# Performance work log

Hardware: AMD Instinct MI355X
Metric: run time of the kernel (lower is better)

## Reference

```python
import jax, jax.numpy as jnp
import numpy as np

N = 50000        # nodes
E = 800000       # edges
H = 256          # hidden_dim == output_dim
L = 5            # num_layers
NUM_ATOM_F = 9   # OGB atom categorical features
NUM_BOND_F = 3   # OGB bond categorical features
ATOM_VOCAB = 64
BOND_VOCAB = 8
G = 128          # num graphs in batch
BN_EPS = 1e-5


def setup_inputs() -> dict:
    key = jax.random.key(0)
    ks = jax.random.split(key, 24)
    s = 0.02
    inp = {
        "x_feat": jax.random.randint(ks[0], (N, NUM_ATOM_F), 0, ATOM_VOCAB),
        "edge_index": jax.random.randint(ks[1], (2, E), 0, N),
        "edge_attr_raw": jax.random.randint(ks[2], (E, NUM_BOND_F), 0, BOND_VOCAB),
        "batch": jnp.sort(jax.random.randint(ks[3], (N,), 0, G)),
        "atom_emb": s * jax.random.normal(ks[4], (NUM_ATOM_F, ATOM_VOCAB, H), jnp.float32),
        "bond_emb": s * jax.random.normal(ks[5], (NUM_BOND_F, BOND_VOCAB, H), jnp.float32),
        # per-layer GINEConv MLP: Linear(H,H) -> BN -> relu -> Linear(H,H) -> relu
        "W1": s * jax.random.normal(ks[6], (L, H, H), jnp.float32),
        "b1": jnp.zeros((L, H), jnp.float32),
        "g1": jnp.ones((L, H), jnp.float32),
        "be1": jnp.zeros((L, H), jnp.float32),
        "W2": s * jax.random.normal(ks[7], (L, H, H), jnp.float32),
        "b2": jnp.zeros((L, H), jnp.float32),
        # outer per-layer BN
        "g2": jnp.ones((L, H), jnp.float32),
        "be2": jnp.zeros((L, H), jnp.float32),
        # output head: Linear -> BN -> relu -> Linear
        "outW1": s * jax.random.normal(ks[8], (H, H), jnp.float32),
        "outb1": jnp.zeros((H,), jnp.float32),
        "outg": jnp.ones((H,), jnp.float32),
        "outbe": jnp.zeros((H,), jnp.float32),
        "outW2": s * jax.random.normal(ks[9], (H, H), jnp.float32),
        "outb2": jnp.zeros((H,), jnp.float32),
    }
    return inp


def _bn(x, g, b):
    mu = jnp.mean(x, axis=0)
    var = jnp.var(x, axis=0)
    return (x - mu) * jax.lax.rsqrt(var + BN_EPS) * g + b


def reference(x_feat, edge_index, edge_attr_raw, batch,
              atom_emb, bond_emb, W1, b1, g1, be1, W2, b2, g2, be2,
              outW1, outb1, outg, outbe, outW2, outb2):
    # Atom/Bond encoders: sum of per-feature embeddings
    x = sum(atom_emb[f][x_feat[:, f]] for f in range(NUM_ATOM_F))        # [N,H]
    e = sum(bond_emb[f][edge_attr_raw[:, f]] for f in range(NUM_BOND_F))  # [E,H]
    src, dst = edge_index[0], edge_index[1]

    for i in range(L):
        # GINEConv: (1+eps)*x + sum_j relu(x_j + e_ij), eps=0
        m = jax.nn.relu(x[src] + e)                       # [E,H]
        agg = jax.ops.segment_sum(m, dst, num_segments=N)  # [N,H]
        h = x + agg
        h = jax.nn.relu(_bn(h @ W1[i] + b1[i], g1[i], be1[i]))
        h = jax.nn.relu(h @ W2[i] + b2[i])
        x = jax.nn.relu(_bn(h, g2[i], be2[i]))

    # output head + global_add_pool
    h = jax.nn.relu(_bn(x @ outW1 + outb1, outg, outbe))
    h = h @ outW2 + outb2
    return jax.ops.segment_sum(h, batch, num_segments=G)   # [G,H]
```

## Files before the change

kernel.cpp:

```cpp
#include <hip/hip_runtime.h>
#include <hip/hip_bf16.h>

#define NN 50000
#define EE 800000
#define HH 256
#define GG 128
#define LL 5
#define NCHUNK 196
#define BN_EPS 1e-5f

typedef __attribute__((ext_vector_type(8))) short short8_t;
typedef __attribute__((ext_vector_type(4))) float f32x4;
typedef __hip_bfloat16 bf16;

#define AS1 __attribute__((address_space(1)))
#define AS3 __attribute__((address_space(3)))

__device__ __forceinline__ float bf2f(unsigned short u) {
    unsigned int i = ((unsigned int)u) << 16;
    float f;
    __builtin_memcpy(&f, &i, 4);
    return f;
}
__device__ __forceinline__ unsigned short f2bf(float f) {
    bf16 h = __float2bfloat16(f);
    unsigned short u;
    __builtin_memcpy(&u, &h, 2);
    return u;
}

__global__ __launch_bounds__(256) void k_encode(const int* __restrict__ xf,
                                                const float* __restrict__ atom_emb,
                                                bf16* __restrict__ x) {
    int n = blockIdx.x, h = threadIdx.x;
    float s = 0.f;
#pragma unroll
    for (int f = 0; f < 9; ++f) {
        int v = xf[n * 9 + f];
        s += atom_emb[((size_t)f * 64 + v) * HH + h];
    }
    x[(size_t)n * HH + h] = __float2bfloat16(s);
}

__global__ __launch_bounds__(256) void k_combo(const float* __restrict__ bond_emb,
                                               bf16* __restrict__ table) {
    int c = blockIdx.x, h = threadIdx.x;
    float v = bond_emb[(size_t)((c >> 6) & 7) * HH + h]
            + bond_emb[(size_t)(8 + ((c >> 3) & 7)) * HH + h]
            + bond_emb[(size_t)(16 + (c & 7)) * HH + h];
    table[(size_t)c * HH + h] = __float2bfloat16(v);
}

__global__ __launch_bounds__(256) void k_prepw(const float* __restrict__ W1,
                                               const float* __restrict__ W2,
                                               const float* __restrict__ oW1,
                                               const float* __restrict__ oW2,
                                               bf16* __restrict__ out) {
    int z = blockIdx.z;
    const float* src = (z < 5) ? W1 + (size_t)z * 65536
                     : (z < 10) ? W2 + (size_t)(z - 5) * 65536
                     : (z == 10) ? oW1 : oW2;
    bf16* dst = out + (size_t)z * 65536;
    __shared__ float tile[32][33];
    int kt = blockIdx.y * 32, nt = blockIdx.x * 32;
    int tx = threadIdx.x, ty = threadIdx.y;
    for (int i = ty; i < 32; i += 8) tile[i][tx] = src[(size_t)(kt + i) * 256 + nt + tx];
    __syncthreads();
    for (int i = ty; i < 32; i += 8)
        dst[(size_t)(nt + i) * 256 + kt + tx] = __float2bfloat16(tile[tx][i]);
}

__global__ __launch_bounds__(256) void k_hist(const int* __restrict__ ei, int* __restrict__ deg) {
    int e = blockIdx.x * 256 + threadIdx.x;
    if (e < EE) atomicAdd(&deg[ei[EE + e]], 1);
}

__global__ __launch_bounds__(256) void k_scan_a(const int* __restrict__ deg, int* __restrict__ ro,
                                                int* __restrict__ bsum) {
    __shared__ int sm[256];
    int b = blockIdx.x, t = threadIdx.x;
    int idx = b * 256 + t;
    int v = (idx < NN) ? deg[idx] : 0;
    sm[t] = v;
    __syncthreads();
    for (int off = 1; off < 256; off <<= 1) {
        int add = (t >= off) ? sm[t - off] : 0;
        __syncthreads();
        sm[t] += add;
        __syncthreads();
    }
    if (idx <= NN) ro[idx] = sm[t] - v;
    if (t == 255) bsum[b] = sm[255];
}

__global__ __launch_bounds__(256) void k_scan_b(int* __restrict__ bsum) {
    __shared__ int sm[256];
    int t = threadIdx.x;
    int v = (t < NCHUNK) ? bsum[t] : 0;
    sm[t] = v;
    __syncthreads();
    for (int off = 1; off < 256; off <<= 1) {
        int add = (t >= off) ? sm[t - off] : 0;
        __syncthreads();
        sm[t] += add;
        __syncthreads();
    }
    if (t < NCHUNK) bsum[t] = sm[t] - v;
}

__global__ __launch_bounds__(256) void k_scan_c(int* __restrict__ ro, const int* __restrict__ bsum,
                                                int* __restrict__ cursor) {
    int b = blockIdx.x, t = threadIdx.x;
    int idx = b * 256 + t;
    if (idx <= NN) {
        int val = ro[idx] + bsum[b];
        ro[idx] = val;
        if (idx < NN) cursor[idx] = val;
    }
}

__global__ __launch_bounds__(256) void k_scatter(const int* __restrict__ ei,
                                                 const int* __restrict__ attr,
                                                 int* __restrict__ cursor,
                                                 int2* __restrict__ ebuf) {
    int e = blockIdx.x * 256 + threadIdx.x;
    if (e < EE) {
        int d = ei[EE + e];
        int c = (attr[e * 3] << 6) | (attr[e * 3 + 1] << 3) | attr[e * 3 + 2];
        int pos = atomicAdd(&cursor[d], 1);
        ebuf[pos] = make_int2(ei[e], c);
    }
}

__global__ __launch_bounds__(256) void k_bnrelu(bf16* __restrict__ t,
                                                const float* __restrict__ sIn,
                                                const float* __restrict__ qIn,
                                                const float* __restrict__ gIn,
                                                const float* __restrict__ beIn,
                                                float invN) {
    int grp = threadIdx.x >> 6;
    int lane = threadIdx.x & 63;
    int h4 = lane * 4;
    float4 s4 = *(const float4*)(sIn + h4);
    float4 q4 = *(const float4*)(qIn + h4);
    float4 g4 = *(const float4*)(gIn + h4);
    float4 b4 = *(const float4*)(beIn + h4);
    float4 cav, cbv;
#define COEF(C)                                                 \
    { float mu = s4.C * invN;                                   \
      float var = fmaf(-mu, mu, q4.C * invN);                   \
      float a = g4.C * rsqrtf(var + BN_EPS);                    \
      cav.C = a; cbv.C = fmaf(-mu, a, b4.C); }
    COEF(x) COEF(y) COEF(z) COEF(w)
#undef COEF
    int n = blockIdx.x * 4 + grp;
    if (n >= NN) return;
    ushort4 v = *(const ushort4*)(t + (size_t)n * HH + h4);
    ushort4 o;
    o.x = f2bf(fmaxf(fmaf(bf2f(v.x), cav.x, cbv.x), 0.f));
    o.y = f2bf(fmaxf(fmaf(bf2f(v.y), cav.y, cbv.y), 0.f));
    o.z = f2bf(fmaxf(fmaf(bf2f(v.z), cav.z, cbv.z), 0.f));
    o.w = f2bf(fmaxf(fmaf(bf2f(v.w), cav.w, cbv.w), 0.f));
    *(ushort4*)(t + (size_t)n * HH + h4) = o;
}

__global__ __launch_bounds__(256) void k_aggregate(const bf16* __restrict__ u,
                                                   const int* __restrict__ ro,
                                                   const int2* __restrict__ eb,
                                                   const bf16* __restrict__ combo,
                                                   bf16* __restrict__ aggout) {
    int wid = threadIdx.x >> 6;
    int lane = threadIdx.x & 63;
    int half = lane >> 5;
    int sl = lane & 31;
    int n = blockIdx.x * 4 + wid;
    if (n >= NN) return;
    int h8 = sl * 8;
    float p0[8] = {0.f, 0.f, 0.f, 0.f, 0.f, 0.f, 0.f, 0.f};
    float p1[8] = {0.f, 0.f, 0.f, 0.f, 0.f, 0.f, 0.f, 0.f};
    int e0 = ro[n], e1 = ro[n + 1];
    int j = e0;
#define ACCUM(P, xs, cs)                                                       \
    {                                                                          \
        unsigned int xw[4] = {xs.x, xs.y, xs.z, xs.w};                         \
        unsigned int cw[4] = {cs.x, cs.y, cs.z, cs.w};                         \
        _Pragma("unroll") for (int q = 0; q < 4; ++q) {                        \
            float xlo = __uint_as_float(xw[q] << 16);                          \
            float xhi = __uint_as_float(xw[q] & 0xffff0000u);                  \
            float clo = __uint_as_float(cw[q] << 16);                          \
            float chi = __uint_as_float(cw[q] & 0xffff0000u);                  \
            P[2 * q] += fmaxf(xlo + clo, 0.f);                                 \
            P[2 * q + 1] += fmaxf(xhi + chi, 0.f);                             \
        }                                                                      \
    }
    for (; j + 4 <= e1; j += 4) {
        int2 rA = eb[j + half];
        int2 rB = eb[j + 2 + half];
        uint4 xA = *(const uint4*)(u + (size_t)rA.x * HH + h8);
        uint4 cA = *(const uint4*)(combo + ((size_t)rA.y << 8) + h8);
        uint4 xB = *(const uint4*)(u + (size_t)rB.x * HH + h8);
        uint4 cB = *(const uint4*)(combo + ((size_t)rB.y << 8) + h8);
        ACCUM(p0, xA, cA);
        ACCUM(p1, xB, cB);
    }
    for (; j < e1; j += 2) {
        int idx = j + half;
        bool v = idx < e1;
        int2 r = eb[v ? idx : e0];
        uint4 xA = *(const uint4*)(u + (size_t)r.x * HH + h8);
        uint4 cA = *(const uint4*)(combo + ((size_t)r.y << 8) + h8);
        if (v) ACCUM(p0, xA, cA);
    }
#undef ACCUM
#pragma unroll
    for (int i = 0; i < 8; ++i) {
        p0[i] += p1[i];
        p0[i] += __shfl_xor(p0[i], 32);
    }
    if (half == 0) {
        uint4 tv = *(const uint4*)(u + (size_t)n * HH + h8);
        unsigned int tw[4] = {tv.x, tv.y, tv.z, tv.w};
        unsigned int ow[4];
#pragma unroll
        for (int q = 0; q < 4; ++q) {
            float tlo = __uint_as_float(tw[q] << 16);
            float thi = __uint_as_float(tw[q] & 0xffff0000u);
            ow[q] = (unsigned int)f2bf(p0[2 * q] + tlo)
                  | ((unsigned int)f2bf(p0[2 * q + 1] + thi) << 16);
        }
        *(uint4*)(aggout + (size_t)n * HH + h8) = make_uint4(ow[0], ow[1], ow[2], ow[3]);
    }
}

struct GLds {
    uint4 a[2][512];
    uint4 b[2][1024];
    float ca[256], cb[256];
};

__device__ __forceinline__ uint4 xchunk(uint4 u, const float* ca, const float* cb, int k0) {
    float4 ca0 = *(const float4*)(ca + k0);
    float4 ca1 = *(const float4*)(ca + k0 + 4);
    float4 cb0 = *(const float4*)(cb + k0);
    float4 cb1 = *(const float4*)(cb + k0 + 4);
    float cav[8] = {ca0.x, ca0.y, ca0.z, ca0.w, ca1.x, ca1.y, ca1.z, ca1.w};
    float cbv[8] = {cb0.x, cb0.y, cb0.z, cb0.w, cb1.x, cb1.y, cb1.z, cb1.w};
    unsigned int s[4] = {u.x, u.y, u.z, u.w};
#pragma unroll
    for (int p = 0; p < 4; ++p) {
        float lo = bf2f((unsigned short)(s[p] & 0xffffu));
        float hi = bf2f((unsigned short)(s[p] >> 16));
        lo = fmaxf(fmaf(lo, cav[2 * p], cbv[2 * p]), 0.f);
        hi = fmaxf(fmaf(hi, cav[2 * p + 1], cbv[2 * p + 1]), 0.f);
        s[p] = (unsigned int)f2bf(lo) | ((unsigned int)f2bf(hi) << 16);
    }
    return make_uint4(s[0], s[1], s[2], s[3]);
}

template <bool HAS_T, bool POOL>
__global__ __launch_bounds__(512, 4) void k_gemm(const bf16* __restrict__ A,
                                                 const bf16* __restrict__ Wt,
                                                 const float* __restrict__ bias,
                                                 bf16* __restrict__ Out,
                                                 int M, int do_relu,
                                                 const float* __restrict__ sIn,
                                                 const float* __restrict__ qIn,
                                                 const float* __restrict__ gIn,
                                                 const float* __restrict__ beIn,
                                                 float invN,
                                                 float* __restrict__ ssum,
                                                 float* __restrict__ ssq,
                                                 const int* __restrict__ pbatch,
                                                 float* __restrict__ pout) {
    __shared__ GLds L;
    const int t = threadIdx.x;
    const int lane = t & 63;
    const int w = t >> 6;
    const int wr = w >> 2, wc = w & 3;
    const int m0 = blockIdx.x * 128;
    const int lhi = lane >> 4, llo = lane & 15;

    if (HAS_T) {
        if (t < 256) {
            float mu = sIn[t] * invN;
            float var = fmaf(-mu, mu, qIn[t] * invN);
            float a = gIn[t] * rsqrtf(var + BN_EPS);
            L.ca[t] = a;
            L.cb[t] = fmaf(-mu, a, beIn[t]);
        }
        __syncthreads();
    }

    const int arow_i = t & 127, akg = t >> 7;
    const bf16* aptr = A + (size_t)(m0 + arow_i) * HH + akg * 8;
    const int bcol = wc * 64 + lane;
    const bf16* bptr = Wt + (size_t)bcol * HH + wr * 8;

    f32x4 acc[4][4] = {};
    uint4 areg, anext;

#define STAGE_B(c, kb)                                                                        \
    _Pragma("unroll") for (int q = 0; q < 2; ++q) {                                           \
        __builtin_amdgcn_global_load_lds((const AS1 void*)(bptr + (kb) + q * 16),             \
                                         (AS3 void*)&L.b[c][q * 512 + w * 64], 16, 0, 0);     \
    }
#define STAGE_A_DMA(c, kb)                                                                    \
    __builtin_amdgcn_global_load_lds((const AS1 void*)(aptr + (kb)),                          \
                                     (AS3 void*)&L.a[c][w * 64], 16, 0, 0);

    STAGE_B(0, 0);
    if (HAS_T) {
        areg = *(const uint4*)(aptr + 0);
        L.a[0][t] = xchunk(areg, L.ca, L.cb, akg * 8);
    } else {
        STAGE_A_DMA(0, 0);
    }
    __syncthreads();

    int c = 0;
    for (int step = 0; step < 8; ++step) {
        const int kn = (step + 1) * 32;
        if (step < 7) {
            STAGE_B(c ^ 1, kn);
            if (HAS_T) anext = *(const uint4*)(aptr + kn);
            else STAGE_A_DMA(c ^ 1, kn);
        }
        short8_t af[4], bfv[4];
#pragma unroll
        for (int m = 0; m < 4; ++m)
            af[m] = *(const short8_t*)&L.a[c][lhi * 128 + wr * 64 + m * 16 + llo];
#pragma unroll
        for (int n = 0; n < 4; ++n)
            bfv[n] = *(const short8_t*)&L.b[c][lhi * 256 + wc * 64 + n * 16 + llo];
#pragma unroll
        for (int m = 0; m < 4; ++m)
#pragma unroll
            for (int n = 0; n < 4; ++n)
                acc[m][n] = __builtin_amdgcn_mfma_f32_16x16x32_bf16(af[m], bfv[n], acc[m][n], 0, 0, 0);
        if (HAS_T && step < 7)
            L.a[c ^ 1][t] = xchunk(anext, L.ca, L.cb, kn + akg * 8);
        __syncthreads();
        c ^= 1;
    }
#undef STAGE_B
#undef STAGE_A_DMA

    float bias_n[4];
    int col_n[4];
#pragma unroll
    for (int n = 0; n < 4; ++n) {
        col_n[n] = wc * 64 + n * 16 + llo;
        bias_n[n] = bias[col_n[n]];
    }

    if (POOL) {
        int gcur = -1;
        float pacc[4] = {0.f, 0.f, 0.f, 0.f};
#pragma unroll
        for (int m = 0; m < 4; ++m) {
#pragma unroll
            for (int j = 0; j < 4; ++j) {
                int row = m0 + wr * 64 + m * 16 + lhi * 4 + j;
                if (row < M) {
                    int g = pbatch[row];
                    if (g != gcur) {
                        if (gcur >= 0) {
#pragma unroll
                            for (int n = 0; n < 4; ++n)
                                atomicAdd(&pout[(size_t)gcur * HH + col_n[n]], pacc[n]);
                        }
                        gcur = g;
#pragma unroll
                        for (int n = 0; n < 4; ++n) pacc[n] = 0.f;
                    }
#pragma unroll
                    for (int n = 0; n < 4; ++n)
                        pacc[n] += acc[m][n][j] + bias_n[n];
                }
            }
        }
        if (gcur >= 0) {
#pragma unroll
            for (int n = 0; n < 4; ++n)
                atomicAdd(&pout[(size_t)gcur * HH + col_n[n]], pacc[n]);
        }
        return;
    }

    float ps[4] = {0.f, 0.f, 0.f, 0.f}, pq[4] = {0.f, 0.f, 0.f, 0.f};
#pragma unroll
    for (int m = 0; m < 4; ++m) {
#pragma unroll
        for (int j = 0; j < 4; ++j) {
            int row = m0 + wr * 64 + m * 16 + lhi * 4 + j;
            bool valid = row < M;
#pragma unroll
            for (int n = 0; n < 4; ++n) {
                float v = acc[m][n][j] + bias_n[n];
                if (do_relu) v = fmaxf(v, 0.f);
                if (valid) {
                    Out[(size_t)row * HH + col_n[n]] = __float2bfloat16(v);
                    ps[n] += v;
                    pq[n] = fmaf(v, v, pq[n]);
                }
            }
        }
    }

    if (ssum) {
#pragma unroll
        for (int n = 0; n < 4; ++n) {
            float s = ps[n];
            s += __shfl_xor(s, 16);
            s += __shfl_xor(s, 32);
            float q = pq[n];
            q += __shfl_xor(q, 16);
            q += __shfl_xor(q, 32);
            if (lhi == 0) {
                atomicAdd(&ssum[col_n[n]], s);
                atomicAdd(&ssq[col_n[n]], q);
            }
        }
    }
}

static size_t align256(size_t v) { return (v + 255) & ~(size_t)255; }

extern "C" void kernel_launch(void* const* d_in, const int* in_sizes, int n_in,
                              void* d_out, int out_size, void* d_ws, size_t ws_size,
                              hipStream_t stream) {
    const int* x_feat = (const int*)d_in[0];
    const int* ei = (const int*)d_in[1];
    const int* attr = (const int*)d_in[2];
    const int* batch = (const int*)d_in[3];
    const float* atom_emb = (const float*)d_in[4];
    const float* bond_emb = (const float*)d_in[5];
    const float* W1 = (const float*)d_in[6];
    const float* b1 = (const float*)d_in[7];
    const float* g1 = (const float*)d_in[8];
    const float* be1 = (const float*)d_in[9];
    const float* W2 = (const float*)d_in[10];
    const float* b2 = (const float*)d_in[11];
    const float* g2 = (const float*)d_in[12];
    const float* be2 = (const float*)d_in[13];
    const float* outW1 = (const float*)d_in[14];
    const float* outb1 = (const float*)d_in[15];
    const float* outg = (const float*)d_in[16];
    const float* outbe = (const float*)d_in[17];
    const float* outW2 = (const float*)d_in[18];
    const float* outb2 = (const float*)d_in[19];
    float* out = (float*)d_out;

    char* ws = (char*)d_ws;
    const size_t BUF_STRIDE = align256((size_t)NN * HH * 2 + 131072);
    bf16* bufA = (bf16*)ws;
    bf16* bufB = (bf16*)(ws + BUF_STRIDE);
    bf16* bufC = (bf16*)(ws + 2 * BUF_STRIDE);
    char* p = ws + 3 * BUF_STRIDE;
    int2* ebuf = (int2*)p;            p += align256((size_t)EE * sizeof(int2));
    int* deg = (int*)p;
    float* stats = (float*)(p + (size_t)NN * sizeof(int));
    const size_t ZERO_BYTES = (size_t)NN * sizeof(int) + 11 * 512 * sizeof(float);
    p += align256(ZERO_BYTES);
    int* ro = (int*)p;                p += align256((size_t)(NN + 1) * sizeof(int));
    int* cursor = (int*)p;            p += align256((size_t)NN * sizeof(int));
    int* bsum = (int*)p;              p += align256(256 * sizeof(int));
    bf16* combo = (bf16*)p;           p += align256((size_t)512 * HH * sizeof(bf16));
    bf16* wbuf = (bf16*)p;            p += align256((size_t)12 * 65536 * sizeof(bf16));

    const float invN = 1.0f / (float)NN;
    const int EBLK = (EE + 255) / 256;
    const int GBLK = (NN + 127) / 128;
    const int AGG_GRID = (NN + 3) / 4;
    const int BNR_GRID = (NN + 3) / 4;

    hipMemsetAsync(deg, 0, ZERO_BYTES, stream);
    hipMemsetAsync(d_out, 0, (size_t)GG * HH * sizeof(float), stream);
    k_hist<<<EBLK, 256, 0, stream>>>(ei, deg);
    k_scan_a<<<NCHUNK, 256, 0, stream>>>(deg, ro, bsum);
    k_scan_b<<<1, 256, 0, stream>>>(bsum);
    k_scan_c<<<NCHUNK, 256, 0, stream>>>(ro, bsum, cursor);
    k_scatter<<<EBLK, 256, 0, stream>>>(ei, attr, cursor, ebuf);
    k_combo<<<512, 256, 0, stream>>>(bond_emb, combo);
    k_prepw<<<dim3(8, 8, 12), dim3(32, 8), 0, stream>>>(W1, W2, outW1, outW2, wbuf);
    k_encode<<<NN, 256, 0, stream>>>(x_feat, atom_emb, bufA);

    for (int l = 0; l < LL; ++l) {
        float* s1 = stats + (size_t)(2 * l) * 512;
        float* q1 = s1 + 256;
        float* s2 = stats + (size_t)(2 * l + 1) * 512;
        float* q2 = s2 + 256;
        if (l > 0) {
            float* sp = stats + (size_t)(2 * l - 1) * 512;
            k_bnrelu<<<BNR_GRID, 256, 0, stream>>>(bufA, sp, sp + 256,
                                                   g2 + (size_t)(l - 1) * HH,
                                                   be2 + (size_t)(l - 1) * HH, invN);
        }
        k_aggregate<<<AGG_GRID, 256, 0, stream>>>(bufA, ro, ebuf, combo, bufB);
        k_gemm<false, false><<<GBLK, 512, 0, stream>>>(bufB, wbuf + (size_t)l * 65536,
                                                       b1 + (size_t)l * HH, bufC, NN, 0,
                                                       nullptr, nullptr, nullptr, nullptr,
                                                       invN, s1, q1, nullptr, nullptr);
        k_gemm<true, false><<<GBLK, 512, 0, stream>>>(bufC, wbuf + (size_t)(5 + l) * 65536,
                                                      b2 + (size_t)l * HH, bufA, NN, 1,
                                                      s1, q1, g1 + (size_t)l * HH,
                                                      be1 + (size_t)l * HH, invN, s2, q2,
                                                      nullptr, nullptr);
    }

    float* sP = stats + (size_t)9 * 512;
    float* sH = stats + (size_t)10 * 512;
    float* qH = sH + 256;
    k_gemm<true, false><<<GBLK, 512, 0, stream>>>(bufA, wbuf + (size_t)10 * 65536, outb1,
                                                  bufB, NN, 0, sP, sP + 256,
                                                  g2 + (size_t)4 * HH, be2 + (size_t)4 * HH,
                                                  invN, sH, qH, nullptr, nullptr);
    k_gemm<true, true><<<GBLK, 512, 0, stream>>>(bufB, wbuf + (size_t)11 * 65536, outb2,
                                                 bufC, NN, 0, sH, qH, outg, outbe,
                                                 invN, nullptr, nullptr, batch, out);
}
```

Baseline: 932.5 us.

## Split GEMM output columns across a second grid dimension with 256-thread blocks

Each GEMM block now computes a 128x128 output tile with 4 waves instead of 128x256 with 8 waves, and a second grid dimension covers the two column halves. This doubles the block count, which gives more parallelism and halves the B tile in LDS, aiming at better occupancy and load balance across CUs. The cost is that each A tile is loaded twice, and the BN transform in HAS_T is recomputed for every column half.

```diff
diff --git a/kernel.cpp b/kernel.cpp
--- a/kernel.cpp
+++ b/kernel.cpp
@@ -234,7 +234,7 @@
 
 struct GLds {
     uint4 a[2][512];
-    uint4 b[2][1024];
+    uint4 b[2][512];
     float ca[256], cb[256];
 };
 
@@ -258,7 +258,7 @@
 }
 
 template <bool HAS_T, bool POOL>
-__global__ __launch_bounds__(512, 4) void k_gemm(const bf16* __restrict__ A,
+__global__ __launch_bounds__(256, 4) void k_gemm(const bf16* __restrict__ A,
                                                  const bf16* __restrict__ Wt,
                                                  const float* __restrict__ bias,
                                                  bf16* __restrict__ Out,
@@ -276,42 +276,73 @@
     const int t = threadIdx.x;
     const int lane = t & 63;
     const int w = t >> 6;
-    const int wr = w >> 2, wc = w & 3;
+    const int wr = w >> 1, wc = w & 1;
     const int m0 = blockIdx.x * 128;
+    const int n0 = blockIdx.y * 128;
     const int lhi = lane >> 4, llo = lane & 15;
 
     if (HAS_T) {
-        if (t < 256) {
-            float mu = sIn[t] * invN;
-            float var = fmaf(-mu, mu, qIn[t] * invN);
-            float a = gIn[t] * rsqrtf(var + BN_EPS);
-            L.ca[t] = a;
-            L.cb[t] = fmaf(-mu, a, beIn[t]);
-        }
+        float mu = sIn[t] * invN;
+        float var = fmaf(-mu, mu, qIn[t] * invN);
+        float a = gIn[t] * rsqrtf(var + BN_EPS);
+        L.ca[t] = a;
+        L.cb[t] = fmaf(-mu, a, beIn[t]);
         __syncthreads();
     }
 
-    const int arow_i = t & 127, akg = t >> 7;
-    const bf16* aptr = A + (size_t)(m0 + arow_i) * HH + akg * 8;
-    const int bcol = wc * 64 + lane;
-    const bf16* bptr = Wt + (size_t)bcol * HH + wr * 8;
+    const int rc = t & 127, kg0 = t >> 7;
+    const bf16* aptr0 = A + (size_t)(m0 + rc) * HH + kg0 * 8;
+    const bf16* aptr1 = aptr0 + 16;
+    const bf16* bptr0 = Wt + (size_t)(n0 + rc) * HH + kg0 * 8;
+    const bf16* bptr1 = bptr0 + 16;
 
     f32x4 acc[4][4] = {};
-    uint4 areg, anext;
+    uint4 ar0, ar1, an0, an1;
 
 #define STAGE_B(c, kb)                                                                        \
-    _Pragma("unroll") for (int q = 0; q < 2; ++q) {                                           \
-        __builtin_amdgcn_global_load_lds((const AS1 void*)(bptr + (kb) + q * 16),             \
-                                         (AS3 void*)&L.b[c][q * 512 + w * 64], 16, 0, 0);     \
+    {                                                                                         \
+        __builtin_amdgcn_global_load_lds((const AS1 void*)(bptr0 + (kb)),                     \
+                                         (AS3 void*)&L.b[c][kg0 * 128 + w * 64], 16, 0, 0);   \
+        __builtin_amdgcn_global_load_lds((const AS1 void*)(bptr1 + (kb)),                     \
+                                         (AS3 void*)&L.b[c][(kg0 + 2) * 128 + w * 64], 16, 0, 0); \
     }
 #define STAGE_A_DMA(c, kb)                                                                    \
-    __builtin_amdgcn_global_load_lds((const AS1 void*)(aptr + (kb)),                          \
-                                     (AS3 void*)&L.a[c][w * 64], 16, 0, 0);
+    {                                                                                         \
+        __builtin_amdgcn_global_load_lds((const AS1 void*)(aptr0 + (kb)),                     \
+                                         (AS3 void*)&L.a[c][kg0 * 128 + w * 64], 16, 0, 0);   \
+        __builtin_amdgcn_global_load_lds((const AS1 void*)(aptr1 + (kb)),                     \
+                                         (AS3 void*)&L.a[c][(kg0 + 2) * 128 + w * 64], 16, 0, 0); \
+    }
+
+#undef STAGE_B
+#undef STAGE_A_DMA
+    const int WBASE = (w & 1) * 64;
+#define STAGE_B(c, kb)                                                                        \
+    {                                                                                         \
+        __builtin_amdgcn_global_load_lds((const AS1 void*)(bptr0 + (kb)),                     \
+                                         (AS3 void*)&L.b[c][kg0 * 128 + WBASE], 16, 0, 0);    \
+        __builtin_amdgcn_global_load_lds((const AS1 void*)(bptr1 + (kb)),                     \
+                                         (AS3 void*)&L.b[c][(kg0 + 2) * 128 + WBASE], 16, 0, 0); \
+    }
+#define STAGE_A_DMA(c, kb)                                                                    \
+    {                                                                                         \
+        __builtin_amdgcn_global_load_lds((const AS1 void*)(aptr0 + (kb)),                     \
+                                         (AS3 void*)&L.a[c][kg0 * 128 + WBASE], 16, 0, 0);    \
+        __builtin_amdgcn_global_load_lds((const AS1 void*)(aptr1 + (kb)),                     \
+                                         (AS3 void*)&L.a[c][(kg0 + 2) * 128 + WBASE], 16, 0, 0); \
+    }
+#define LOAD_A(kb)  { an0 = *(const uint4*)(aptr0 + (kb)); an1 = *(const uint4*)(aptr1 + (kb)); }
+#define WRITE_A(c, kb)                                                                        \
+    {                                                                                         \
+        L.a[c][kg0 * 128 + rc] = xchunk(ar0, L.ca, L.cb, (kb) + kg0 * 8);                     \
+        L.a[c][(kg0 + 2) * 128 + rc] = xchunk(ar1, L.ca, L.cb, (kb) + (kg0 + 2) * 8);         \
+    }
 
     STAGE_B(0, 0);
     if (HAS_T) {
-        areg = *(const uint4*)(aptr + 0);
-        L.a[0][t] = xchunk(areg, L.ca, L.cb, akg * 8);
+        ar0 = *(const uint4*)(aptr0 + 0);
+        ar1 = *(const uint4*)(aptr1 + 0);
+        WRITE_A(0, 0);
     } else {
         STAGE_A_DMA(0, 0);
     }
@@ -322,7 +353,7 @@
         const int kn = (step + 1) * 32;
         if (step < 7) {
             STAGE_B(c ^ 1, kn);
-            if (HAS_T) anext = *(const uint4*)(aptr + kn);
+            if (HAS_T) LOAD_A(kn)
             else STAGE_A_DMA(c ^ 1, kn);
         }
         short8_t af[4], bfv[4];
@@ -331,25 +362,30 @@
             af[m] = *(const short8_t*)&L.a[c][lhi * 128 + wr * 64 + m * 16 + llo];
 #pragma unroll
         for (int n = 0; n < 4; ++n)
-            bfv[n] = *(const short8_t*)&L.b[c][lhi * 256 + wc * 64 + n * 16 + llo];
+            bfv[n] = *(const short8_t*)&L.b[c][lhi * 128 + wc * 64 + n * 16 + llo];
 #pragma unroll
         for (int m = 0; m < 4; ++m)
 #pragma unroll
             for (int n = 0; n < 4; ++n)
                 acc[m][n] = __builtin_amdgcn_mfma_f32_16x16x32_bf16(af[m], bfv[n], acc[m][n], 0, 0, 0);
-        if (HAS_T && step < 7)
-            L.a[c ^ 1][t] = xchunk(anext, L.ca, L.cb, kn + akg * 8);
+        if (HAS_T && step < 7) {
+            ar0 = an0;
+            ar1 = an1;
+            WRITE_A(c ^ 1, kn);
+        }
         __syncthreads();
         c ^= 1;
     }
 #undef STAGE_B
 #undef STAGE_A_DMA
+#undef LOAD_A
+#undef WRITE_A
 
     float bias_n[4];
     int col_n[4];
 #pragma unroll
     for (int n = 0; n < 4; ++n) {
-        col_n[n] = wc * 64 + n * 16 + llo;
+        col_n[n] = n0 + wc * 64 + n * 16 + llo;
         bias_n[n] = bias[col_n[n]];
     }
 
@@ -470,7 +506,7 @@
 
     const float invN = 1.0f / (float)NN;
     const int EBLK = (EE + 255) / 256;
-    const int GBLK = (NN + 127) / 128;
+    const dim3 GGRID((NN + 127) / 128, 2);
     const int AGG_GRID = (NN + 3) / 4;
     const int BNR_GRID = (NN + 3) / 4;
 
@@ -497,25 +533,25 @@
                                                    be2 + (size_t)(l - 1) * HH, invN);
         }
         k_aggregate<<<AGG_GRID, 256, 0, stream>>>(bufA, ro, ebuf, combo, bufB);
-        k_gemm<false, false><<<GBLK, 512, 0, stream>>>(bufB, wbuf + (size_t)l * 65536,
-                                                       b1 + (size_t)l * HH, bufC, NN, 0,
-                                                       nullptr, nullptr, nullptr, nullptr,
-                                                       invN, s1, q1, nullptr, nullptr);
-        k_gemm<true, false><<<GBLK, 512, 0, stream>>>(bufC, wbuf + (size_t)(5 + l) * 65536,
-                                                      b2 + (size_t)l * HH, bufA, NN, 1,
-                                                      s1, q1, g1 + (size_t)l * HH,
-                                                      be1 + (size_t)l * HH, invN, s2, q2,
-                                                      nullptr, nullptr);
+        k_gemm<false, false><<<GGRID, 256, 0, stream>>>(bufB, wbuf + (size_t)l * 65536,
+                                                        b1 + (size_t)l * HH, bufC, NN, 0,
+                                                        nullptr, nullptr, nullptr, nullptr,
+                                                        invN, s1, q1, nullptr, nullptr);
+        k_gemm<true, false><<<GGRID, 256, 0, stream>>>(bufC, wbuf + (size_t)(5 + l) * 65536,
+                                                       b2 + (size_t)l * HH, bufA, NN, 1,
+                                                       s1, q1, g1 + (size_t)l * HH,
+                                                       be1 + (size_t)l * HH, invN, s2, q2,
+                                                       nullptr, nullptr);
     }
 
     float* sP = stats + (size_t)9 * 512;
     float* sH = stats + (size_t)10 * 512;
     float* qH = sH + 256;
-    k_gemm<true, false><<<GBLK, 512, 0, stream>>>(bufA, wbuf + (size_t)10 * 65536, outb1,
-                                                  bufB, NN, 0, sP, sP + 256,
-                                                  g2 + (size_t)4 * HH, be2 + (size_t)4 * HH,
-                                                  invN, sH, qH, nullptr, nullptr);
-    k_gemm<true, true><<<GBLK, 512, 0, stream>>>(bufB, wbuf + (size_t)11 * 65536, outb2,
-                                                 bufC, NN, 0, sH, qH, outg, outbe,
-                                                 invN, nullptr, nullptr, batch, out);
-}
+    k_gemm<true, false><<<GGRID, 256, 0, stream>>>(bufA, wbuf + (size_t)10 * 65536, outb1,
+                                                   bufB, NN, 0, sP, sP + 256,
+                                                   g2 + (size_t)4 * HH, be2 + (size_t)4 * HH,
+                                                   invN, sH, qH, nullptr, nullptr);
+    k_gemm<true, true><<<GGRID, 256, 0, stream>>>(bufB, wbuf + (size_t)11 * 65536, outb2,
+                                                  bufC, NN, 0, sH, qH, outg, outbe,
+                                                  invN, nullptr, nullptr, batch, out);
+}
```

New measurement: 1.029 ms. 10.4% more time.
